# Optimization experiments

Hardware: AMD Instinct MI355X
Metric: run time of the kernel (lower is better)

Reference implementation:

```python
import jax, jax.numpy as jnp
import numpy as np

H_SIZE = 1024
N_HEADS = 16
HEAD_DIM = H_SIZE // N_HEADS
TAU2 = 1.0
LN_EPS = 1e-5


def setup_inputs() -> dict:
    key = jax.random.key(0)
    ks = jax.random.split(key, 12)
    B, S = 2, 1024
    s = 1.0 / np.sqrt(H_SIZE)
    inp = {
        "input": jax.random.normal(ks[0], (B, S, H_SIZE), dtype=jnp.float32),
        "input_mask": jnp.ones((B, S), dtype=jnp.float32),
        # uniform(0,1) noise; converted to Gumbel(0,1) inside reference
        "gumbel": jax.random.uniform(ks[1], (B, N_HEADS, S, S), dtype=jnp.float32,
                                     minval=1e-10, maxval=1.0),
        "Wq": jax.random.normal(ks[2], (H_SIZE, H_SIZE), dtype=jnp.float32) * s,
        "bq": jnp.zeros((H_SIZE,), dtype=jnp.float32),
        "Wk": jax.random.normal(ks[3], (H_SIZE, H_SIZE), dtype=jnp.float32) * s,
        "bk": jnp.zeros((H_SIZE,), dtype=jnp.float32),
        "Wv": jax.random.normal(ks[4], (H_SIZE, H_SIZE), dtype=jnp.float32) * s,
        "bv": jnp.zeros((H_SIZE,), dtype=jnp.float32),
        "Wo": jax.random.normal(ks[5], (H_SIZE, H_SIZE), dtype=jnp.float32) * s,
        "bo": jnp.zeros((H_SIZE,), dtype=jnp.float32),
        "gamma": jnp.ones((H_SIZE,), dtype=jnp.float32),
        "beta": jnp.zeros((H_SIZE,), dtype=jnp.float32),
    }
    return inp


def reference(input, input_mask, gumbel, Wq, bq, Wk, bk, Wv, bv, Wo, bo, gamma, beta):
    B, S, _ = input.shape
    # projections -> [B, H, S, D]
    def proj(W, b):
        y = jnp.einsum('bsh,oh->bso', input, W) + b  # torch Linear: x @ W.T + b
        return y.reshape(B, S, N_HEADS, HEAD_DIM).transpose(0, 2, 1, 3)
    qq = proj(Wq, bq)
    kk = proj(Wk, bk)
    vv = proj(Wv, bv)
    # raw scores (NOTE: original has no 1/sqrt(d) scaling)
    interact = jnp.einsum('bhqd,bhkd->bhqk', qq, kk)
    # gumbel-softmax (soft): softmax((logits + g)/tau)
    g = -jnp.log(-jnp.log(gumbel))
    sto_attn = jax.nn.softmax((interact + g) / TAU2, axis=-1)
    # masking: mask_1 over query dim, mask_2 over key dim
    mask = input_mask[:, None, :, None] * input_mask[:, None, None, :]  # [B,1,S,S]
    attn = sto_attn * mask
    # (dropout p=0 -> identity)
    out = jnp.einsum('bhqk,bhkd->bhqd', attn, vv)
    out = out.transpose(0, 2, 1, 3).reshape(B, S, H_SIZE)
    out = jnp.einsum('bsh,oh->bso', out, Wo) + bo
    # residual + layernorm
    x = out + input
    mu = jnp.mean(x, axis=-1, keepdims=True)
    var = jnp.mean(jnp.square(x - mu), axis=-1, keepdims=True)
    return (x - mu) * jax.lax.rsqrt(var + LN_EPS) * gamma + beta
```

## Files before the change

### kernel.cpp

```cpp
#include <hip/hip_runtime.h>

#define S_LEN 1024
#define HSZ   1024
#define NHEAD 16
#define HD    64
#define BATCH 2
#define MROWS 2048
#define LOG2E 1.4426950408889634f
#define M0L2  72.134752044448f

typedef unsigned short u16;
typedef __attribute__((ext_vector_type(8))) short short8;
typedef __attribute__((ext_vector_type(4))) short short4v;
typedef __attribute__((ext_vector_type(4))) float f32x4;

#define MFMA_BF16(a, b, c) __builtin_amdgcn_mfma_f32_16x16x32_bf16((a), (b), (c), 0, 0, 0)

__device__ __forceinline__ u16 f2bf(float f) {
    union { float f; unsigned u; } c; c.f = f;
    unsigned u = c.u;
    u += 0x7fffu + ((u >> 16) & 1u);
    return (u16)(u >> 16);
}
__device__ __forceinline__ float bf2f(u16 s) {
    union { unsigned u; float f; } c; c.u = ((unsigned)s) << 16;
    return c.f;
}
__device__ __forceinline__ short8 ld8(const u16* p) {
    return *reinterpret_cast<const short8*>(p);
}
__device__ __forceinline__ void gld16(const u16* g, u16* l) {
    __builtin_amdgcn_global_load_lds(
        (const __attribute__((address_space(1))) unsigned int*)g,
        (__attribute__((address_space(3))) unsigned int*)l, 16, 0, 0);
}
__device__ __forceinline__ int frag_off(int row, int cbb) {
    return (((row << 3) | (cbb ^ (row & 7))) << 3);
}
__device__ __forceinline__ int frag_off16(int row, int cbb) {
    return (((row << 4) | (cbb ^ (row & 15))) << 3);
}

template<int MT>
__device__ __forceinline__ void gemm_tile(const u16* __restrict__ Ag,
                                          const u16* __restrict__ Bg,
                                          int klen, u16* As, u16* Bs,
                                          f32x4 (&acc)[MT][4]) {
    const int tid  = threadIdx.x;
    const int wave = tid >> 6, lane = tid & 63;
    const int lr = lane & 15, grp = lane >> 4;
    const int wm = wave >> 1, wn = wave & 1;

#pragma unroll
    for (int mt = 0; mt < MT; mt++)
#pragma unroll
        for (int nt = 0; nt < 4; nt++)
            acc[mt][nt] = (f32x4){0.f, 0.f, 0.f, 0.f};

    for (int k0 = 0; k0 < klen; k0 += 128) {
        __syncthreads();
#pragma unroll
        for (int j = 0; j < 2 * MT; j++) {
            int c = j * 256 + tid, row = c >> 4, cb = (c & 15) ^ (row & 15);
            gld16(Ag + (size_t)row * HSZ + k0 + cb * 8, As + c * 8);
        }
#pragma unroll
        for (int j = 0; j < 8; j++) {
            int c = j * 256 + tid, row = c >> 4, cb = (c & 15) ^ (row & 15);
            gld16(Bg + (size_t)row * HSZ + k0 + cb * 8, Bs + c * 8);
        }
        __syncthreads();

#pragma unroll
        for (int h = 0; h < 4; h++) {
            const int cbb = h * 4 + grp;
            short8 af[MT], bf[4];
#pragma unroll
            for (int mt = 0; mt < MT; mt++)
                af[mt] = ld8(As + frag_off16(wm * (MT * 16) + mt * 16 + lr, cbb));
#pragma unroll
            for (int nt = 0; nt < 4; nt++)
                bf[nt] = ld8(Bs + frag_off16(wn * 64 + nt * 16 + lr, cbb));
#pragma unroll
            for (int mt = 0; mt < MT; mt++)
#pragma unroll
                for (int nt = 0; nt < 4; nt++)
                    acc[mt][nt] = MFMA_BF16(af[mt], bf[nt], acc[mt][nt]);
        }
    }
}

__global__ __launch_bounds__(256)
void convert_kernel(const float* __restrict__ x,  const float* __restrict__ wq,
                    const float* __restrict__ wk, const float* __restrict__ wv,
                    const float* __restrict__ wo, u16* __restrict__ dst) {
    const int XV = (MROWS * HSZ) / 4;
    const int WV = (HSZ * HSZ) / 4;
    int vid = blockIdx.x * 256 + threadIdx.x;
    const float* src; int off;
    if (vid < XV)            { src = x;  off = vid; }
    else if (vid < XV + WV)  { src = wq; off = vid - XV; }
    else if (vid < XV + 2*WV){ src = wk; off = vid - XV - WV; }
    else if (vid < XV + 3*WV){ src = wv; off = vid - XV - 2*WV; }
    else                     { src = wo; off = vid - XV - 3*WV; }
    float4 v = reinterpret_cast<const float4*>(src)[off];
    ushort4 o;
    o.x = f2bf(v.x); o.y = f2bf(v.y); o.z = f2bf(v.z); o.w = f2bf(v.w);
    reinterpret_cast<ushort4*>(dst)[vid] = o;
}

__global__ __launch_bounds__(256)
void qkv_gemm(const u16* __restrict__ xb,
              const u16* __restrict__ wqb, const u16* __restrict__ wkb,
              const u16* __restrict__ wvb,
              const float* __restrict__ bq, const float* __restrict__ bk,
              const float* __restrict__ bv, const float* __restrict__ mask,
              u16* __restrict__ qout, u16* __restrict__ kout,
              u16* __restrict__ vtout) {
    __shared__ u16 As[64 * 128];
    __shared__ u16 Bs[128 * 128];
    const int ntile = blockIdx.x;
    const int mtile = blockIdx.y;
    const int p  = ntile >> 3;
    const int m0 = mtile * 64;
    const int nw = (ntile & 7) * 128;
    const u16*  W    = (p == 0) ? wqb : (p == 1) ? wkb : wvb;
    const float* bias = (p == 0) ? bq : (p == 1) ? bk : bv;

    f32x4 acc[2][4];
    gemm_tile<2>(xb + (size_t)m0 * HSZ, W + (size_t)nw * HSZ, HSZ, As, Bs, acc);

    const int wave = threadIdx.x >> 6, lane = threadIdx.x & 63;
    const int lr = lane & 15, grp = lane >> 4;
    const int wm = wave >> 1, wn = wave & 1;
#pragma unroll
    for (int mt = 0; mt < 2; mt++)
#pragma unroll
        for (int nt = 0; nt < 4; nt++)
#pragma unroll
            for (int r = 0; r < 4; r++) {
                int m = m0 + wm * 32 + mt * 16 + grp * 4 + r;
                int o = nw + wn * 64 + nt * 16 + lr;
                float val = acc[mt][nt][r] + bias[o];
                int b = m >> 10, s = m & 1023, hh = o >> 6, d = o & 63;
                if (p == 0)
                    qout[(((size_t)(b * NHEAD + hh)) * S_LEN + s) * HD + d] = f2bf(val);
                else if (p == 1)
                    kout[(((size_t)(b * NHEAD + hh)) * S_LEN + s) * HD + d] = f2bf(val);
                else
                    vtout[(((size_t)(b * NHEAD + hh)) * HD + d) * S_LEN + s] =
                        f2bf(val * mask[m]);
            }
}

__global__ __launch_bounds__(256, 4)
void attn_kernel(const u16* __restrict__ qb, const u16* __restrict__ kb,
                 const u16* __restrict__ vt, const float* __restrict__ gumbel,
                 u16* __restrict__ po, float* __restrict__ pl) {
    const int bh   = blockIdx.y;
    const int qt   = blockIdx.x;
    const int half = blockIdx.z;
    const int q0 = qt * 64, kbase = half * 512;
    const int tid = threadIdx.x;
    const int wave = tid >> 6, lane = tid & 63;
    const int lr = lane & 15, grp = lane >> 4;

    const u16* Q = qb + (size_t)bh * S_LEN * HD;
    const u16* K = kb + (size_t)bh * S_LEN * HD;
    const u16* V = vt + (size_t)bh * HD * S_LEN;
    const float* G = gumbel + (size_t)bh * S_LEN * S_LEN;
    const int qw = q0 + wave * 16;

    __shared__ u16 Ks[64 * 64];
    __shared__ u16 Vs[64 * 64];
    __shared__ u16 pbuf[4 * 16 * 68];

    u16* pw = pbuf + wave * (16 * 68);

    short8 aq0 = ld8(Q + (size_t)(qw + lr) * HD + grp * 8);
    short8 aq1 = ld8(Q + (size_t)(qw + lr) * HD + 32 + grp * 8);

    short8 ones;
#pragma unroll
    for (int j = 0; j < 8; j++) ones[j] = (short)0x3F80;

    f32x4 acco[4];
#pragma unroll
    for (int i = 0; i < 4; i++) acco[i] = (f32x4){0.f, 0.f, 0.f, 0.f};
    f32x4 accl = (f32x4){0.f, 0.f, 0.f, 0.f};

    const float* Grow[4];
#pragma unroll
    for (int r = 0; r < 4; r++)
        Grow[r] = G + (size_t)(qw + grp * 4 + r) * S_LEN + lr;

    float gpre[4][4];
#pragma unroll
    for (int kt = 0; kt < 4; kt++)
#pragma unroll
        for (int r = 0; r < 4; r++)
            gpre[kt][r] = Grow[r][kbase + kt * 16];

    for (int it = 0; it < 8; it++) {
        const int k0 = kbase + it * 64;
        __syncthreads();
#pragma unroll
        for (int j = 0; j < 2; j++) {
            int c = j * 256 + tid, row = c >> 3, cb = (c & 7) ^ (row & 7);
            gld16(K + (size_t)(k0 + row) * HD + cb * 8, Ks + c * 8);
        }
#pragma unroll
        for (int j = 0; j < 2; j++) {
            int c = j * 256 + tid, row = c >> 3, cb = (c & 7) ^ (row & 7);
            gld16(V + (size_t)row * S_LEN + k0 + cb * 8, Vs + c * 8);
        }
        float w[4][4];
#pragma unroll
        for (int kt = 0; kt < 4; kt++)
#pragma unroll
            for (int r = 0; r < 4; r++)
                w[kt][r] = __builtin_amdgcn_rcpf(__builtin_amdgcn_logf(gpre[kt][r]));
        __syncthreads();

        if (it < 7) {
#pragma unroll
            for (int kt = 0; kt < 4; kt++)
#pragma unroll
                for (int r = 0; r < 4; r++)
                    gpre[kt][r] = Grow[r][k0 + 64 + kt * 16];
        }

        float sc[4][4];
#pragma unroll
        for (int kt = 0; kt < 4; kt++) {
            int row = kt * 16 + lr;
            f32x4 a = (f32x4){0.f, 0.f, 0.f, 0.f};
            a = MFMA_BF16(aq0, ld8(Ks + frag_off(row, grp)), a);
            a = MFMA_BF16(aq1, ld8(Ks + frag_off(row, 4 + grp)), a);
#pragma unroll
            for (int r = 0; r < 4; r++) sc[kt][r] = a[r];
        }

#pragma unroll
        for (int kt = 0; kt < 4; kt++)
#pragma unroll
            for (int r = 0; r < 4; r++) {
                float e = __builtin_amdgcn_exp2f(fmaf(sc[kt][r], LOG2E, -M0L2));
                pw[(grp * 4 + r) * 68 + kt * 16 + lr] = f2bf(e * w[kt][r]);
            }

        short8 pa[2];
#pragma unroll
        for (int ks = 0; ks < 2; ks++) {
            const u16* pp = pw + lr * 68 + ks * 32 + grp * 8;
            short4v lo = *reinterpret_cast<const short4v*>(pp);
            short4v hi = *reinterpret_cast<const short4v*>(pp + 4);
            pa[ks] = __builtin_shufflevector(lo, hi, 0, 1, 2, 3, 4, 5, 6, 7);
        }

#pragma unroll
        for (int nt = 0; nt < 4; nt++) {
            int row = nt * 16 + lr;
#pragma unroll
            for (int ks = 0; ks < 2; ks++)
                acco[nt] = MFMA_BF16(pa[ks], ld8(Vs + frag_off(row, ks * 4 + grp)),
                                     acco[nt]);
        }
#pragma unroll
        for (int ks = 0; ks < 2; ks++)
            accl = MFMA_BF16(pa[ks], ones, accl);
    }

    const int qidx = ((half * 32 + bh) * 16 + qt) * 64 + wave * 16 + grp * 4;
    if (lr == 0) {
#pragma unroll
        for (int r = 0; r < 4; r++) pl[qidx + r] = accl[r];
    }
#pragma unroll
    for (int nt = 0; nt < 4; nt++)
#pragma unroll
        for (int r = 0; r < 4; r++)
            po[(size_t)(qidx + r) * 64 + nt * 16 + lr] = f2bf(acco[nt][r]);
}

__global__ __launch_bounds__(256)
void combine_kernel(const u16* __restrict__ po, const float* __restrict__ pl,
                    const float* __restrict__ mask, u16* __restrict__ ctx) {
    const int qt = blockIdx.x, bh = blockIdx.y;
    const int b = bh >> 4, h = bh & 15;
    const int q = threadIdx.x >> 2;
    const int dc = (threadIdx.x & 3) * 16;
    const int i0 = ((0 * 32 + bh) * 16 + qt) * 64 + q;
    const int i1 = ((1 * 32 + bh) * 16 + qt) * 64 + q;
    float l = pl[i0] + pl[i1];
    float mq = mask[b * S_LEN + qt * 64 + q] / l;
    u16* dst = ctx + ((size_t)(b * S_LEN + qt * 64 + q)) * HSZ + h * 64 + dc;
#pragma unroll
    for (int c = 0; c < 2; c++) {
        short8 a = ld8(po + (size_t)i0 * 64 + dc + c * 8);
        short8 bm = ld8(po + (size_t)i1 * 64 + dc + c * 8);
        short8 o;
#pragma unroll
        for (int j = 0; j < 8; j++)
            o[j] = (short)f2bf((bf2f((u16)a[j]) + bf2f((u16)bm[j])) * mq);
        *reinterpret_cast<short8*>(dst + c * 8) = o;
    }
}

__global__ __launch_bounds__(256)
void oproj_gemm(const u16* __restrict__ A, const u16* __restrict__ W,
                float* __restrict__ part0, float* __restrict__ part1) {
    __shared__ u16 As[64 * 128];
    __shared__ u16 Bs[128 * 128];
    const int ntile = blockIdx.x;
    const int mtile = blockIdx.y;
    const int z     = blockIdx.z;
    const int m0 = mtile * 64, n0 = ntile * 128, koff = z * 512;

    f32x4 acc[2][4];
    gemm_tile<2>(A + (size_t)m0 * HSZ + koff, W + (size_t)n0 * HSZ + koff,
                 512, As, Bs, acc);

    float* dst = z ? part1 : part0;
    const int wave = threadIdx.x >> 6, lane = threadIdx.x & 63;
    const int lr = lane & 15, grp = lane >> 4;
    const int wm = wave >> 1, wn = wave & 1;
#pragma unroll
    for (int mt = 0; mt < 2; mt++)
#pragma unroll
        for (int nt = 0; nt < 4; nt++)
#pragma unroll
            for (int r = 0; r < 4; r++) {
                int m = m0 + wm * 32 + mt * 16 + grp * 4 + r;
                int o = n0 + wn * 64 + nt * 16 + lr;
                dst[(size_t)m * HSZ + o] = acc[mt][nt][r];
            }
}

__global__ __launch_bounds__(256)
void ln_kernel(const float* __restrict__ part0, const float* __restrict__ part1,
               const float* __restrict__ xin, const float* __restrict__ bo,
               const float* __restrict__ gamma, const float* __restrict__ beta,
               float* __restrict__ out) {
    const int row = blockIdx.x;
    const int tid = threadIdx.x;
    const size_t base = (size_t)row * (HSZ / 4);

    float4 p0 = reinterpret_cast<const float4*>(part0)[base + tid];
    float4 p1 = reinterpret_cast<const float4*>(part1)[base + tid];
    float4 xr = reinterpret_cast<const float4*>(xin)[base + tid];
    float4 bb = reinterpret_cast<const float4*>(bo)[tid];
    float4 v;
    v.x = p0.x + p1.x + xr.x + bb.x;
    v.y = p0.y + p1.y + xr.y + bb.y;
    v.z = p0.z + p1.z + xr.z + bb.z;
    v.w = p0.w + p1.w + xr.w + bb.w;

    float s  = v.x + v.y + v.z + v.w;
    float ss = v.x * v.x + v.y * v.y + v.z * v.z + v.w * v.w;
#pragma unroll
    for (int off = 1; off < 64; off <<= 1) {
        s  += __shfl_xor(s, off, 64);
        ss += __shfl_xor(ss, off, 64);
    }
    __shared__ float red[8];
    int wave = tid >> 6, lane = tid & 63;
    if (lane == 0) { red[wave] = s; red[4 + wave] = ss; }
    __syncthreads();
    s  = red[0] + red[1] + red[2] + red[3];
    ss = red[4] + red[5] + red[6] + red[7];
    float mu  = s * (1.f / HSZ);
    float var = ss * (1.f / HSZ) - mu * mu;
    float rstd = rsqrtf(var + 1e-5f);

    float4 g  = reinterpret_cast<const float4*>(gamma)[tid];
    float4 be = reinterpret_cast<const float4*>(beta)[tid];
    float4 o;
    o.x = (v.x - mu) * rstd * g.x + be.x;
    o.y = (v.y - mu) * rstd * g.y + be.y;
    o.z = (v.z - mu) * rstd * g.z + be.z;
    o.w = (v.w - mu) * rstd * g.w + be.w;
    reinterpret_cast<float4*>(out)[base + tid] = o;
}

extern "C" void kernel_launch(void* const* d_in, const int* in_sizes, int n_in,
                              void* d_out, int out_size, void* d_ws, size_t ws_size,
                              hipStream_t stream) {
    (void)in_sizes; (void)n_in; (void)out_size; (void)ws_size;
    const float* x     = (const float*)d_in[0];
    const float* mask  = (const float*)d_in[1];
    const float* gum   = (const float*)d_in[2];
    const float* Wq    = (const float*)d_in[3];
    const float* bq    = (const float*)d_in[4];
    const float* Wk    = (const float*)d_in[5];
    const float* bk    = (const float*)d_in[6];
    const float* Wv    = (const float*)d_in[7];
    const float* bv    = (const float*)d_in[8];
    const float* Wo    = (const float*)d_in[9];
    const float* bo    = (const float*)d_in[10];
    const float* gamma = (const float*)d_in[11];
    const float* beta  = (const float*)d_in[12];
    float* out = (float*)d_out;

    u16* xb  = (u16*)d_ws;
    u16* wqb = xb  + 2097152;
    u16* wkb = wqb + 1048576;
    u16* wvb = wkb + 1048576;
    u16* wob = wvb + 1048576;
    u16* qb  = wob + 1048576;
    u16* kb  = qb  + 2097152;
    u16* vt  = kb  + 2097152;
    u16* ctx = vt  + 2097152;
    float* part0 = (float*)(ctx + 2097152);
    float* pl    = (float*)((char*)part0 + 8388608);
    u16*   po    = xb;
    float* part1 = (float*)xb;

    convert_kernel<<<dim3(6144), dim3(256), 0, stream>>>(x, Wq, Wk, Wv, Wo, xb);
    qkv_gemm<<<dim3(24, 32), dim3(256), 0, stream>>>(xb, wqb, wkb, wvb,
                                                     bq, bk, bv, mask,
                                                     qb, kb, vt);
    attn_kernel<<<dim3(16, 32, 2), dim3(256), 0, stream>>>(qb, kb, vt, gum, po, pl);
    combine_kernel<<<dim3(16, 32), dim3(256), 0, stream>>>(po, pl, mask, ctx);
    oproj_gemm<<<dim3(8, 32, 2), dim3(256), 0, stream>>>(ctx, wob, part0, part1);
    ln_kernel<<<dim3(2048), dim3(256), 0, stream>>>(part0, part1, x, bo,
                                                    gamma, beta, out);
}
```

Before: 289.0 us.

## Split key range across waves in-block and fuse the combine step into attention

Each attention block now covers 32 queries over the full key range. Pairs of waves split each 128-key tile and merge their partial outputs and row sums through shared memory. This removes the separate combine kernel and the global round-trip of bf16 partial outputs and row sums, and it writes the normalised, masked context directly. In exchange, the block uses more LDS (about 41 KB), adds extra barriers, drops the occupancy hint from launch bounds, and loads larger K/V tiles with a 16-column swizzle.

```diff
diff --git a/kernel.cpp b/kernel.cpp
--- a/kernel.cpp
+++ b/kernel.cpp
@@ -153,27 +153,30 @@
             }
 }
 
-__global__ __launch_bounds__(256, 4)
+__global__ __launch_bounds__(256)
 void attn_kernel(const u16* __restrict__ qb, const u16* __restrict__ kb,
                  const u16* __restrict__ vt, const float* __restrict__ gumbel,
-                 u16* __restrict__ po, float* __restrict__ pl) {
-    const int bh   = blockIdx.y;
-    const int qt   = blockIdx.x;
-    const int half = blockIdx.z;
-    const int q0 = qt * 64, kbase = half * 512;
+                 const float* __restrict__ mask, u16* __restrict__ ctx) {
+    const int bh = blockIdx.y;
+    const int b = bh >> 4, h = bh & 15;
+    const int qt = blockIdx.x;
     const int tid = threadIdx.x;
     const int wave = tid >> 6, lane = tid & 63;
     const int lr = lane & 15, grp = lane >> 4;
+    const int wq2 = wave >> 1, kp = wave & 1;
 
     const u16* Q = qb + (size_t)bh * S_LEN * HD;
     const u16* K = kb + (size_t)bh * S_LEN * HD;
     const u16* V = vt + (size_t)bh * HD * S_LEN;
     const float* G = gumbel + (size_t)bh * S_LEN * S_LEN;
-    const int qw = q0 + wave * 16;
-
-    __shared__ u16 Ks[64 * 64];
-    __shared__ u16 Vs[64 * 64];
-    __shared__ u16 pbuf[4 * 16 * 68];
+    const int qw = qt * 32 + wq2 * 16;
+
+    __shared__ __align__(16) char smem[41472];
+    u16* Ks   = (u16*)smem;
+    u16* Vs   = (u16*)(smem + 16384);
+    u16* pbuf = (u16*)(smem + 32768);
+    float* comb = (float*)smem;
+    float* la   = (float*)(smem + 8192);
 
     u16* pw = pbuf + wave * (16 * 68);
 
@@ -192,27 +195,27 @@
     const float* Grow[4];
 #pragma unroll
     for (int r = 0; r < 4; r++)
-        Grow[r] = G + (size_t)(qw + grp * 4 + r) * S_LEN + lr;
+        Grow[r] = G + (size_t)(qw + grp * 4 + r) * S_LEN + kp * 64 + lr;
 
     float gpre[4][4];
 #pragma unroll
     for (int kt = 0; kt < 4; kt++)
 #pragma unroll
         for (int r = 0; r < 4; r++)
-            gpre[kt][r] = Grow[r][kbase + kt * 16];
-
-    for (int it = 0; it < 8; it++) {
-        const int k0 = kbase + it * 64;
+            gpre[kt][r] = Grow[r][kt * 16];
+
+    for (int j = 0; j < 8; j++) {
+        const int k0 = j * 128;
         __syncthreads();
 #pragma unroll
-        for (int j = 0; j < 2; j++) {
-            int c = j * 256 + tid, row = c >> 3, cb = (c & 7) ^ (row & 7);
+        for (int i = 0; i < 4; i++) {
+            int c = i * 256 + tid, row = c >> 3, cb = (c & 7) ^ (row & 7);
             gld16(K + (size_t)(k0 + row) * HD + cb * 8, Ks + c * 8);
         }
 #pragma unroll
-        for (int j = 0; j < 2; j++) {
-            int c = j * 256 + tid, row = c >> 3, cb = (c & 7) ^ (row & 7);
-            gld16(V + (size_t)row * S_LEN + k0 + cb * 8, Vs + c * 8);
+        for (int i = 0; i < 4; i++) {
+            int c = i * 256 + tid, row = c >> 4, cc = (c & 15) ^ (row & 15);
+            gld16(V + (size_t)row * S_LEN + k0 + cc * 8, Vs + c * 8);
         }
         float w[4][4];
 #pragma unroll
@@ -222,21 +225,21 @@
                 w[kt][r] = __builtin_amdgcn_rcpf(__builtin_amdgcn_logf(gpre[kt][r]));
         __syncthreads();
 
-        if (it < 7) {
+        if (j < 7) {
 #pragma unroll
             for (int kt = 0; kt < 4; kt++)
 #pragma unroll
                 for (int r = 0; r < 4; r++)
-                    gpre[kt][r] = Grow[r][k0 + 64 + kt * 16];
+                    gpre[kt][r] = Grow[r][k0 + 128 + kt * 16];
         }
 
         float sc[4][4];
 #pragma unroll
         for (int kt = 0; kt < 4; kt++) {
-            int row = kt * 16 + lr;
+            int krow = kp * 64 + kt * 16 + lr;
             f32x4 a = (f32x4){0.f, 0.f, 0.f, 0.f};
-            a = MFMA_BF16(aq0, ld8(Ks + frag_off(row, grp)), a);
-            a = MFMA_BF16(aq1, ld8(Ks + frag_off(row, 4 + grp)), a);
+            a = MFMA_BF16(aq0, ld8(Ks + frag_off(krow, grp)), a);
+            a = MFMA_BF16(aq1, ld8(Ks + frag_off(krow, 4 + grp)), a);
 #pragma unroll
             for (int r = 0; r < 4; r++) sc[kt][r] = a[r];
         }
@@ -260,10 +263,11 @@
 
 #pragma unroll
         for (int nt = 0; nt < 4; nt++) {
-            int row = nt * 16 + lr;
+            int vrow = nt * 16 + lr;
 #pragma unroll
             for (int ks = 0; ks < 2; ks++)
-                acco[nt] = MFMA_BF16(pa[ks], ld8(Vs + frag_off(row, ks * 4 + grp)),
+                acco[nt] = MFMA_BF16(pa[ks],
+                                     ld8(Vs + frag_off16(vrow, kp * 8 + ks * 4 + grp)),
                                      acco[nt]);
         }
 #pragma unroll
@@ -271,39 +275,36 @@
             accl = MFMA_BF16(pa[ks], ones, accl);
     }
 
-    const int qidx = ((half * 32 + bh) * 16 + qt) * 64 + wave * 16 + grp * 4;
-    if (lr == 0) {
-#pragma unroll
-        for (int r = 0; r < 4; r++) pl[qidx + r] = accl[r];
+    __syncthreads();
+    if (kp == 1) {
+#pragma unroll
+        for (int nt = 0; nt < 4; nt++)
+#pragma unroll
+            for (int r = 0; r < 4; r++)
+                comb[wq2 * 1024 + (grp * 4 + r) * 64 + nt * 16 + lr] = acco[nt][r];
+        if (lr == 0) {
+#pragma unroll
+            for (int r = 0; r < 4; r++) la[wq2 * 16 + grp * 4 + r] = accl[r];
+        }
     }
-#pragma unroll
-    for (int nt = 0; nt < 4; nt++)
-#pragma unroll
-        for (int r = 0; r < 4; r++)
-            po[(size_t)(qidx + r) * 64 + nt * 16 + lr] = f2bf(acco[nt][r]);
-}
-
-__global__ __launch_bounds__(256)
-void combine_kernel(const u16* __restrict__ po, const float* __restrict__ pl,
-                    const float* __restrict__ mask, u16* __restrict__ ctx) {
-    const int qt = blockIdx.x, bh = blockIdx.y;
-    const int b = bh >> 4, h = bh & 15;
-    const int q = threadIdx.x >> 2;
-    const int dc = (threadIdx.x & 3) * 16;
-    const int i0 = ((0 * 32 + bh) * 16 + qt) * 64 + q;
-    const int i1 = ((1 * 32 + bh) * 16 + qt) * 64 + q;
-    float l = pl[i0] + pl[i1];
-    float mq = mask[b * S_LEN + qt * 64 + q] / l;
-    u16* dst = ctx + ((size_t)(b * S_LEN + qt * 64 + q)) * HSZ + h * 64 + dc;
-#pragma unroll
-    for (int c = 0; c < 2; c++) {
-        short8 a = ld8(po + (size_t)i0 * 64 + dc + c * 8);
-        short8 bm = ld8(po + (size_t)i1 * 64 + dc + c * 8);
-        short8 o;
-#pragma unroll
-        for (int j = 0; j < 8; j++)
-            o[j] = (short)f2bf((bf2f((u16)a[j]) + bf2f((u16)bm[j])) * mq);
-        *reinterpret_cast<short8*>(dst + c * 8) = o;
+    __syncthreads();
+    if (kp == 0) {
+        float mq[4];
+#pragma unroll
+        for (int r = 0; r < 4; r++) {
+            float l = accl[r] + la[wq2 * 16 + grp * 4 + r];
+            mq[r] = mask[b * S_LEN + qw + grp * 4 + r] / l;
+        }
+#pragma unroll
+        for (int nt = 0; nt < 4; nt++)
+#pragma unroll
+            for (int r = 0; r < 4; r++) {
+                int q = qw + grp * 4 + r;
+                float val = acco[nt][r] +
+                            comb[wq2 * 1024 + (grp * 4 + r) * 64 + nt * 16 + lr];
+                ctx[((size_t)(b * S_LEN + q)) * HSZ + h * 64 + nt * 16 + lr] =
+                    f2bf(val * mq[r]);
+            }
     }
 }
 
@@ -412,16 +413,13 @@
     u16* vt  = kb  + 2097152;
     u16* ctx = vt  + 2097152;
     float* part0 = (float*)(ctx + 2097152);
-    float* pl    = (float*)((char*)part0 + 8388608);
-    u16*   po    = xb;
     float* part1 = (float*)xb;
 
     convert_kernel<<<dim3(6144), dim3(256), 0, stream>>>(x, Wq, Wk, Wv, Wo, xb);
     qkv_gemm<<<dim3(24, 32), dim3(256), 0, stream>>>(xb, wqb, wkb, wvb,
                                                      bq, bk, bv, mask,
                                                      qb, kb, vt);
-    attn_kernel<<<dim3(16, 32, 2), dim3(256), 0, stream>>>(qb, kb, vt, gum, po, pl);
-    combine_kernel<<<dim3(16, 32), dim3(256), 0, stream>>>(po, pl, mask, ctx);
+    attn_kernel<<<dim3(32, 32), dim3(256), 0, stream>>>(qb, kb, vt, gum, mask, ctx);
     oproj_gemm<<<dim3(8, 32, 2), dim3(256), 0, stream>>>(ctx, wob, part0, part1);
     ln_kernel<<<dim3(2048), dim3(256), 0, stream>>>(part0, part1, x, bo,
                                                     gamma, beta, out);
```

Result: no change. 291.5 us (+0.9%).
